# Kernel tuning notes

Measured on AMD Instinct MI355X. Metric: run time of the kernel, lower is better.

Reference implementation:

```python
import math
import jax, jax.numpy as jnp
import numpy as np

# Dimensions (scalar irreps: o3.Irreps('8x0e').dim == 8, FullyConnectedTensorProduct
# between scalar irreps reduces to a learned bilinear map with a 3D weight tensor)
N = 50000       # nodes
C = 4           # channel dim ('c' in the einsum 'nci,neio->nceo')
DI = 8          # irreps_in.dim
DE = 8          # irreps_edge_attr.dim (must equal DI for the einsum to typecheck)
DO = 8          # irreps_out.dim (must equal DI for lin2 to consume the messages)
DA = 16         # irreps_node_attr.dim
E = 400000      # edges
F_EDGE = 32     # number_of_edge_features
H = 64          # radial_neurons
NUM_NEIGHBORS = 8


def setup_inputs() -> dict:
    key = jax.random.key(0)
    ks = jax.random.split(key, 12)
    inv = lambda f: 1.0 / np.sqrt(f)
    return {
        "node_input": jax.random.normal(ks[0], (N, C, DI), jnp.float32),
        "node_attr": jax.random.normal(ks[1], (N, DA), jnp.float32),
        "edge_features": jax.random.normal(ks[2], (E, F_EDGE), jnp.float32),
        # bilinear tensor-product weights (sc, lin1, lin2)
        "W_sc": jax.random.normal(ks[3], (DI, DA, DO), jnp.float32) * inv(DI * DA),
        "W_lin1": jax.random.normal(ks[4], (DI, DA, DI), jnp.float32) * inv(DI * DA),
        "W_lin2": jax.random.normal(ks[5], (DO, DA, DO), jnp.float32) * inv(DO * DA),
        # radial MLP: Linear(F_EDGE,H) -> SiLU -> Linear(H, DI*DE*DO)
        "fc_w1": jax.random.normal(ks[6], (F_EDGE, H), jnp.float32) * inv(F_EDGE),
        "fc_b1": jnp.zeros((H,), jnp.float32),
        "fc_w2": jax.random.normal(ks[7], (H, DI * DE * DO), jnp.float32) * inv(H),
        "fc_b2": jnp.zeros((DI * DE * DO,), jnp.float32),
        "edge_src": jax.random.randint(ks[8], (E,), 0, N, jnp.int32),
        "edge_dst": jax.random.randint(ks[9], (E,), 0, N, jnp.int32),
    }


def reference(node_input, node_attr, edge_features, W_sc, W_lin1, W_lin2,
              fc_w1, fc_b1, fc_w2, fc_b2, edge_src, edge_dst):
    n_nodes = node_input.shape[0]
    # self-connection and input linear (bilinear in node feature & node attr)
    s = jnp.einsum('nci,na,iao->nco', node_input, node_attr, W_sc)      # [N,C,DO]
    x = jnp.einsum('nci,na,iaj->ncj', node_input, node_attr, W_lin1)    # [N,C,DI]
    # radial MLP -> per-edge weight tensor [E, DI, DE, DO]
    h = jax.nn.silu(edge_features @ fc_w1 + fc_b1)
    ef = (h @ fc_w2 + fc_b2).reshape(-1, DI, DE, DO)
    # gather by source, per-edge contraction (einsum 'nci,neio->nceo'):
    # contract x's irrep dim with ef axis 2, keep ef axis 1 as output dim d
    msg = jnp.einsum('eci,edio->ecdo', x[edge_src], ef)                 # [E,C,DI,DO]
    # scatter-add to destination nodes
    agg = jax.ops.segment_sum(msg, edge_dst, num_segments=n_nodes)      # [N,C,DI,DO]
    agg = agg / jnp.sqrt(jnp.asarray(NUM_NEIGHBORS, agg.dtype))
    # output linear on the last (irreps_out) axis
    x2 = jnp.einsum('ncdo,na,oap->ncdp', agg, node_attr, W_lin2)        # [N,C,DI,DO]
    c_s = math.sin(math.pi / 8.0)
    # fully-connected scalar-irrep TP -> output_mask is all ones -> c_x scalar
    c_x = math.cos(math.pi / 8.0)
    return c_s * s[:, :, None, :] + c_x * x2
```

## Files before the change

kernel.cpp:

```cpp
#include <hip/hip_runtime.h>
#include <math.h>

#define CC 4
#define FE 32
#define HH 64
#define EBS 256
#define KEXT 544
#define ASTR 69

typedef __attribute__((ext_vector_type(8))) short bf16x8;
typedef __attribute__((ext_vector_type(4))) float f32x4;

__device__ inline unsigned short f2bf(float f) {
    unsigned u = __float_as_uint(f);
    u += 0x7fffu + ((u >> 16) & 1u);
    return (unsigned short)(u >> 16);
}
__device__ inline float bf2f(unsigned short b) {
    return __uint_as_float(((unsigned)b) << 16);
}

__global__ __launch_bounds__(256) void k_nodeprep(
    const float* __restrict__ node_input, const float* __restrict__ node_attr,
    const float* __restrict__ W_lin1, const float* __restrict__ W_sc,
    const float* __restrict__ W_lin2,
    float* __restrict__ xbuf, float* __restrict__ sbuf,
    float* __restrict__ w2n_ws, int N)
{
    const float c_s = 0.3826834323650898f;
    const float c_x_scaled = 0.9238795325112867f * 0.35355339059327373f;
    int node = blockIdx.x * 4 + (threadIdx.x >> 6);
    int lane = threadIdx.x & 63;
    if (node >= N) return;

    float attr_own = (lane < 16) ? node_attr[(size_t)node * 16 + lane] : 0.f;
    float ni_own   = (lane < 32) ? node_input[(size_t)node * 32 + lane] : 0.f;

    int iw = lane >> 3, jw = lane & 7;
    float wb1 = 0.f, wbs = 0.f, w2n = 0.f;
    #pragma unroll
    for (int a = 0; a < 16; ++a) {
        float fa = __shfl(attr_own, a);
        int idx = (iw * 16 + a) * 8 + jw;
        wb1 += fa * W_lin1[idx];
        wbs += fa * W_sc[idx];
        w2n += fa * W_lin2[idx];
    }
    w2n_ws[(size_t)node * 64 + lane] = c_x_scaled * w2n;

    int c_ = (lane >> 3) & 3, jo = lane & 7;
    float xo = 0.f, so = 0.f;
    #pragma unroll
    for (int i = 0; i < 8; ++i) {
        float niv = __shfl(ni_own, c_ * 8 + i);
        xo += niv * __shfl(wb1, i * 8 + jo);
        so += niv * __shfl(wbs, i * 8 + jo);
    }
    if (lane < 32) {
        xbuf[(size_t)node * 32 + lane] = xo;
        sbuf[(size_t)node * 32 + lane] = c_s * so;
    }
}

__global__ __launch_bounds__(256) void k_hist(
    const int* __restrict__ edge_dst, int* __restrict__ counts, int E)
{
    int e = blockIdx.x * 256 + threadIdx.x;
    if (e < E) atomicAdd(&counts[edge_dst[e]], 1);
}

__global__ __launch_bounds__(1024) void k_scanA(
    const int* __restrict__ counts, int* __restrict__ offsets,
    int* __restrict__ btot, int N)
{
    __shared__ int wsum[16];
    __shared__ int wpre[16];
    int tid = threadIdx.x, wid = tid >> 6, lane = tid & 63;
    int idx = blockIdx.x * 1024 + tid;
    int v = (idx < N) ? counts[idx] : 0;
    int x = v;
    #pragma unroll
    for (int s = 1; s < 64; s <<= 1) {
        int y = __shfl_up(x, s);
        if (lane >= s) x += y;
    }
    if (lane == 63) wsum[wid] = x;
    __syncthreads();
    if (wid == 0) {
        int wv = (lane < 16) ? wsum[lane] : 0;
        int wx = wv;
        #pragma unroll
        for (int s = 1; s < 16; s <<= 1) {
            int y = __shfl_up(wx, s);
            if (lane >= s) wx += y;
        }
        if (lane < 16) wpre[lane] = wx - wv;
    }
    __syncthreads();
    int excl = wpre[wid] + (x - v);
    if (idx < N) offsets[idx] = excl;
    if (tid == 1023) btot[blockIdx.x] = excl + v;
}

__global__ __launch_bounds__(1024) void k_scanB(int* __restrict__ btot, int nb)
{
    __shared__ int wsum[16];
    __shared__ int wpre[16];
    int tid = threadIdx.x, wid = tid >> 6, lane = tid & 63;
    int v = (tid < nb) ? btot[tid] : 0;
    int x = v;
    #pragma unroll
    for (int s = 1; s < 64; s <<= 1) {
        int y = __shfl_up(x, s);
        if (lane >= s) x += y;
    }
    if (lane == 63) wsum[wid] = x;
    __syncthreads();
    if (wid == 0) {
        int wv = (lane < 16) ? wsum[lane] : 0;
        int wx = wv;
        #pragma unroll
        for (int s = 1; s < 16; s <<= 1) {
            int y = __shfl_up(wx, s);
            if (lane >= s) wx += y;
        }
        if (lane < 16) wpre[lane] = wx - wv;
    }
    __syncthreads();
    if (tid < nb) btot[tid] = wpre[wid] + (x - v);
}

__global__ __launch_bounds__(256) void k_scanC(
    int* __restrict__ offsets, const int* __restrict__ btot,
    int* __restrict__ cursor, int N)
{
    int i = blockIdx.x * 256 + threadIdx.x;
    if (i < N) {
        int o = offsets[i] + btot[i >> 10];
        offsets[i] = o;
        cursor[i] = o;
    }
}

__global__ __launch_bounds__(256) void k_fill(
    const int* __restrict__ edge_dst, const int* __restrict__ edge_src,
    int* __restrict__ cursor, int* __restrict__ srcs, int* __restrict__ epos, int E)
{
    int e = blockIdx.x * 256 + threadIdx.x;
    if (e < E) {
        int pos = atomicAdd(&cursor[edge_dst[e]], 1);
        srcs[pos] = edge_src[e];
        epos[e] = pos;
    }
}

__global__ __launch_bounds__(256) void k_prep_bfrag(
    const float* __restrict__ fc_w2, const float* __restrict__ fc_b2,
    unsigned short* __restrict__ Bfrag)
{
    int t = blockIdx.x * 256 + threadIdx.x;
    if (t >= KEXT * 64) return;
    int kappa = t >> 6, nu = t & 63;
    int d = nu >> 3, o = nu & 7;
    float val;
    if (kappa < 512)      val = fc_w2[(size_t)(kappa >> 3) * 512 + d * 64 + (kappa & 7) * 8 + o];
    else if (kappa < 520) val = fc_b2[d * 64 + (kappa & 7) * 8 + o];
    else                  val = 0.f;
    int kk = kappa >> 5;
    int lane = ((kappa >> 3) & 3) * 16 + (nu & 15);
    int ct = nu >> 4;
    int j = kappa & 7;
    Bfrag[(size_t)((kk * 4 + ct) * 64 + lane) * 8 + j] = f2bf(val);
}

__global__ __launch_bounds__(256) void k_prep_bfrag1(
    const float* __restrict__ fc_w1, unsigned short* __restrict__ Bfrag1)
{
    int t = blockIdx.x * 256 + threadIdx.x;
    if (t >= 4 * 64 * 8) return;
    int j = t & 7, l = (t >> 3) & 63, ct = t >> 9;
    int k = (l >> 4) * 8 + j;
    int n = ct * 16 + (l & 15);
    Bfrag1[t] = f2bf(fc_w1[(size_t)k * HH + n]);
}

__global__ __launch_bounds__(256) void k_hsilu(
    const float* __restrict__ edge_features,
    const unsigned short* __restrict__ Bfrag1, const float* __restrict__ fc_b1,
    const int* __restrict__ epos,
    unsigned short* __restrict__ H, int E)
{
    int wid = threadIdx.x >> 6, lane = threadIdx.x & 63;
    int e0 = (blockIdx.x * 4 + wid) * 16;
    if (e0 >= E) return;

    bf16x8 b[4];
    #pragma unroll
    for (int ct = 0; ct < 4; ++ct) {
        uint4 bv = reinterpret_cast<const uint4*>(Bfrag1)[ct * 64 + lane];
        b[ct] = *reinterpret_cast<bf16x8*>(&bv);
    }
    float bias[4];
    #pragma unroll
    for (int ct = 0; ct < 4; ++ct) bias[ct] = fc_b1[ct * 16 + (lane & 15)];

    int pr[4];
    #pragma unroll
    for (int v = 0; v < 4; ++v) {
        int r = e0 + (lane >> 4) * 4 + v;
        pr[v] = (r < E) ? epos[r] : -1;
    }

    int row = e0 + (lane & 15);
    if (row >= E) row = E - 1;
    const float4* ap = reinterpret_cast<const float4*>(
        edge_features + (size_t)row * FE + (lane >> 4) * 8);
    float4 a0 = ap[0], a1 = ap[1];
    unsigned au[4];
    au[0] = (unsigned)f2bf(a0.x) | ((unsigned)f2bf(a0.y) << 16);
    au[1] = (unsigned)f2bf(a0.z) | ((unsigned)f2bf(a0.w) << 16);
    au[2] = (unsigned)f2bf(a1.x) | ((unsigned)f2bf(a1.y) << 16);
    au[3] = (unsigned)f2bf(a1.z) | ((unsigned)f2bf(a1.w) << 16);
    bf16x8 a = *reinterpret_cast<bf16x8*>(au);

    f32x4 acc[4];
    #pragma unroll
    for (int ct = 0; ct < 4; ++ct) {
        acc[ct] = (f32x4){0.f, 0.f, 0.f, 0.f};
        acc[ct] = __builtin_amdgcn_mfma_f32_16x16x32_bf16(a, b[ct], acc[ct], 0, 0, 0);
    }

    #pragma unroll
    for (int ct = 0; ct < 4; ++ct) {
        #pragma unroll
        for (int v = 0; v < 4; ++v) {
            if (pr[v] >= 0) {
                float x = acc[ct][v] + bias[ct];
                float s = x / (1.f + __expf(-x));
                H[(size_t)pr[v] * HH + ct * 16 + (lane & 15)] = f2bf(s);
            }
        }
    }
}

__global__ __launch_bounds__(256) void k_zgemm(
    const unsigned short* __restrict__ H, const int* __restrict__ srcs,
    const int* __restrict__ offsets, const int* __restrict__ counts,
    const float* __restrict__ xin, const unsigned short* __restrict__ Bfrag,
    const float* __restrict__ sbuf, const float* __restrict__ w2n_ws,
    float* __restrict__ out, int N)
{
    __shared__ uint4 alds[16 * ASTR];
    int wid = threadIdx.x >> 6, lane = threadIdx.x & 63;
    int node = blockIdx.x * 4 + wid;
    bool valid = (node < N);

    float z[CC][8];
    #pragma unroll
    for (int c = 0; c < CC; ++c)
        #pragma unroll
        for (int i = 0; i < 8; ++i) z[c][i] = 0.f;
    float xsown = 0.f;

    int off = 0, cnt = 0;
    if (valid) { off = offsets[node]; cnt = counts[node]; }
    for (int base = 0; base < cnt; base += 64) {
        int m = (cnt - base < 64) ? (cnt - base) : 64;
        int sj = (lane < m) ? srcs[off + base + lane] : 0;
        #pragma unroll 2
        for (int j = 0; j < m; ++j) {
            int src = __shfl(sj, j);
            float hk = bf2f(H[(size_t)(off + base + j) * HH + lane]);
            const float4* xp = reinterpret_cast<const float4*>(xin + (size_t)src * 32);
            float xs[32];
            #pragma unroll
            for (int q = 0; q < 8; ++q) {
                float4 v = xp[q];
                xs[q * 4 + 0] = v.x; xs[q * 4 + 1] = v.y;
                xs[q * 4 + 2] = v.z; xs[q * 4 + 3] = v.w;
            }
            #pragma unroll
            for (int c = 0; c < CC; ++c)
                #pragma unroll
                for (int i = 0; i < 8; ++i)
                    z[c][i] += hk * xs[c * 8 + i];
            xsown += xin[(size_t)src * 32 + (lane & 31)];
        }
    }

    #pragma unroll
    for (int c = 0; c < CC; ++c) {
        uint4 pk;
        pk.x = (unsigned)f2bf(z[c][0]) | ((unsigned)f2bf(z[c][1]) << 16);
        pk.y = (unsigned)f2bf(z[c][2]) | ((unsigned)f2bf(z[c][3]) << 16);
        pk.z = (unsigned)f2bf(z[c][4]) | ((unsigned)f2bf(z[c][5]) << 16);
        pk.w = (unsigned)f2bf(z[c][6]) | ((unsigned)f2bf(z[c][7]) << 16);
        alds[(wid * 4 + c) * ASTR + lane] = pk;
    }
    float xb[8];
    #pragma unroll
    for (int i = 0; i < 8; ++i) xb[i] = __shfl(xsown, (lane & 3) * 8 + i);
    int r4 = wid * 4;
    if (lane < 4) {
        uint4 pk;
        pk.x = (unsigned)f2bf(xb[0]) | ((unsigned)f2bf(xb[1]) << 16);
        pk.y = (unsigned)f2bf(xb[2]) | ((unsigned)f2bf(xb[3]) << 16);
        pk.z = (unsigned)f2bf(xb[4]) | ((unsigned)f2bf(xb[5]) << 16);
        pk.w = (unsigned)f2bf(xb[6]) | ((unsigned)f2bf(xb[7]) << 16);
        alds[(r4 + lane) * ASTR + 64] = pk;
    } else if (lane < 16) {
        int j = lane - 4;
        uint4 zz; zz.x = 0u; zz.y = 0u; zz.z = 0u; zz.w = 0u;
        alds[(r4 + (j & 3)) * ASTR + 65 + (j >> 2)] = zz;
    }

    bf16x8 bfr[17];
    #pragma unroll
    for (int kk = 0; kk < 16; ++kk) {
        uint4 bv = reinterpret_cast<const uint4*>(Bfrag)[(kk * 4 + wid) * 64 + lane];
        bfr[kk] = *reinterpret_cast<bf16x8*>(&bv);
    }
    {
        uint4 bv = reinterpret_cast<const uint4*>(Bfrag)[(64 + wid) * 64 + lane];
        bfr[16] = *reinterpret_cast<bf16x8*>(&bv);
    }

    __syncthreads();

    f32x4 acc = (f32x4){0.f, 0.f, 0.f, 0.f};
    #pragma unroll
    for (int kk = 0; kk < 16; ++kk) {
        uint4 av = alds[(lane & 15) * ASTR + kk * 4 + (lane >> 4)];
        bf16x8 a = *reinterpret_cast<bf16x8*>(&av);
        acc = __builtin_amdgcn_mfma_f32_16x16x32_bf16(a, bfr[kk], acc, 0, 0, 0);
    }
    {
        uint4 av = alds[(lane & 15) * ASTR + 64 + (lane >> 4)];
        bf16x8 a = *reinterpret_cast<bf16x8*>(&av);
        acc = __builtin_amdgcn_mfma_f32_16x16x32_bf16(a, bfr[16], acc, 0, 0, 0);
    }

    int q = lane >> 4;
    int colc = lane & 15;
    int nq = blockIdx.x * 4 + q;
    bool vq = (nq < N);
    int realn = vq ? nq : 0;
    int col = wid * 16 + colc;
    int p = col & 7;
    int dloc8 = (colc >> 3) << 3;
    float w2r[8];
    #pragma unroll
    for (int o = 0; o < 8; ++o)
        w2r[o] = vq ? w2n_ws[(size_t)realn * 64 + o * 8 + p] : 0.f;
    #pragma unroll
    for (int v = 0; v < 4; ++v) {
        float res = 0.f;
        #pragma unroll
        for (int o = 0; o < 8; ++o)
            res += __shfl(acc[v], q * 16 + dloc8 + o) * w2r[o];
        if (vq) {
            float sv = sbuf[(size_t)realn * 32 + v * 8 + p];
            out[(size_t)(realn * 4 + v) * 64 + col] = sv + res;
        }
    }
}

__global__ __launch_bounds__(256) void k_node_out(
    const float* __restrict__ sbuf, const float* __restrict__ w2n_ws,
    float* __restrict__ out, int N)
{
    int node = blockIdx.x * 4 + (threadIdx.x >> 6);
    int lane = threadIdx.x & 63;
    if (node >= N) return;
    int d = lane >> 3, p = lane & 7;

    float w2 = w2n_ws[(size_t)node * 64 + lane];
    float s_own = sbuf[(size_t)node * 32 + (lane & 31)];

    float w2sh[8];
    #pragma unroll
    for (int o = 0; o < 8; ++o) w2sh[o] = __shfl(w2, o * 8 + p);

    float* rowp = out + (size_t)node * 256;
    #pragma unroll
    for (int c = 0; c < CC; ++c) {
        float a_own = rowp[c * 64 + lane];
        float res = 0.f;
        #pragma unroll
        for (int o = 0; o < 8; ++o)
            res += __shfl(a_own, d * 8 + o) * w2sh[o];
        float sval = __shfl(s_own, c * 8 + p);
        rowp[c * 64 + lane] = sval + res;
    }
}

__global__ __launch_bounds__(EBS) void k_edge_atomic(
    const float* __restrict__ edge_features,
    const float* __restrict__ fc_w1, const float* __restrict__ fc_b1,
    const float* __restrict__ fc_w2, const float* __restrict__ fc_b2,
    const int* __restrict__ edge_src, const int* __restrict__ edge_dst,
    const float* __restrict__ xin, float* __restrict__ agg, int E)
{
    __shared__ float hlds[HH * EBS];
    int e = blockIdx.x * EBS + threadIdx.x;
    if (e >= E) return;
    float h[HH];
    #pragma unroll
    for (int k = 0; k < HH; ++k) h[k] = fc_b1[k];
    const float4* efp = reinterpret_cast<const float4*>(edge_features + (size_t)e * FE);
    #pragma unroll
    for (int fq = 0; fq < FE / 4; ++fq) {
        float4 efv = efp[fq];
        float ev[4] = {efv.x, efv.y, efv.z, efv.w};
        #pragma unroll
        for (int fs = 0; fs < 4; ++fs) {
            float evv = ev[fs];
            const float4* w1p = reinterpret_cast<const float4*>(fc_w1 + (fq * 4 + fs) * HH);
            #pragma unroll
            for (int q = 0; q < HH / 4; ++q) {
                float4 w = w1p[q];
                h[q * 4 + 0] += evv * w.x;
                h[q * 4 + 1] += evv * w.y;
                h[q * 4 + 2] += evv * w.z;
                h[q * 4 + 3] += evv * w.w;
            }
        }
    }
    #pragma unroll
    for (int k = 0; k < HH; ++k) {
        float v = h[k];
        hlds[k * EBS + threadIdx.x] = v / (1.f + __expf(-v));
    }
    int src = edge_src[e], dst = edge_dst[e];
    float xs[32];
    const float4* xp = reinterpret_cast<const float4*>(xin + (size_t)src * 32);
    #pragma unroll
    for (int q = 0; q < 8; ++q) {
        float4 v = xp[q];
        xs[q * 4 + 0] = v.x; xs[q * 4 + 1] = v.y;
        xs[q * 4 + 2] = v.z; xs[q * 4 + 3] = v.w;
    }
    float* outp = agg + (size_t)dst * 256;
    #pragma unroll 1
    for (int d = 0; d < 8; ++d) {
        float t[64];
        const float4* b2p = reinterpret_cast<const float4*>(fc_b2 + d * 64);
        #pragma unroll
        for (int q = 0; q < 16; ++q) {
            float4 v = b2p[q];
            t[q * 4 + 0] = v.x; t[q * 4 + 1] = v.y;
            t[q * 4 + 2] = v.z; t[q * 4 + 3] = v.w;
        }
        for (int k = 0; k < HH; ++k) {
            float hv = hlds[k * EBS + threadIdx.x];
            const float4* wp = reinterpret_cast<const float4*>(fc_w2 + (size_t)k * 512 + d * 64);
            #pragma unroll
            for (int q = 0; q < 16; ++q) {
                float4 w = wp[q];
                t[q * 4 + 0] += hv * w.x;
                t[q * 4 + 1] += hv * w.y;
                t[q * 4 + 2] += hv * w.z;
                t[q * 4 + 3] += hv * w.w;
            }
        }
        #pragma unroll
        for (int c = 0; c < CC; ++c) {
            #pragma unroll
            for (int o = 0; o < 8; ++o) {
                float acc = 0.f;
                #pragma unroll
                for (int i = 0; i < 8; ++i) acc += xs[c * 8 + i] * t[i * 8 + o];
                atomicAdd(outp + c * 64 + d * 8 + o, acc);
            }
        }
    }
}

extern "C" void kernel_launch(void* const* d_in, const int* in_sizes, int n_in,
                              void* d_out, int out_size, void* d_ws, size_t ws_size,
                              hipStream_t stream)
{
    const float* node_input    = (const float*)d_in[0];
    const float* node_attr     = (const float*)d_in[1];
    const float* edge_features = (const float*)d_in[2];
    const float* W_sc          = (const float*)d_in[3];
    const float* W_lin1        = (const float*)d_in[4];
    const float* W_lin2        = (const float*)d_in[5];
    const float* fc_w1         = (const float*)d_in[6];
    const float* fc_b1         = (const float*)d_in[7];
    const float* fc_w2         = (const float*)d_in[8];
    const float* fc_b2         = (const float*)d_in[9];
    const int*   edge_src      = (const int*)d_in[10];
    const int*   edge_dst      = (const int*)d_in[11];

    const int N = in_sizes[1] / 16;
    const int E = in_sizes[10];
    const int nb = (N + 1023) / 1024;

    char* ws = (char*)d_ws;
    size_t off = 0;
    auto take = [&](size_t bytes) { char* p = ws + off; off += (bytes + 15) & ~(size_t)15; return p; };
    float* xbuf            = (float*)take((size_t)N * 32 * sizeof(float));
    float* sbuf            = (float*)take((size_t)N * 32 * sizeof(float));
    float* w2n_ws          = (float*)take((size_t)N * 64 * sizeof(float));
    int*   counts          = (int*)take((size_t)N * sizeof(int));
    int*   offsets         = (int*)take((size_t)N * sizeof(int));
    int*   cursor          = (int*)take((size_t)N * sizeof(int));
    int*   btot            = (int*)take((size_t)1024 * sizeof(int));
    int*   srcs            = (int*)take((size_t)E * sizeof(int));
    int*   epos            = (int*)take((size_t)E * sizeof(int));
    unsigned short* Bfrag  = (unsigned short*)take((size_t)17 * 4 * 64 * 8 * sizeof(unsigned short));
    unsigned short* Bfrag1 = (unsigned short*)take((size_t)4 * 64 * 8 * sizeof(unsigned short));
    unsigned short* Hbuf   = (unsigned short*)take((size_t)E * HH * sizeof(unsigned short));
    bool fast = (off <= ws_size);

    float* out = (float*)d_out;

    k_nodeprep<<<(N + 3) / 4, 256, 0, stream>>>(
        node_input, node_attr, W_lin1, W_sc, W_lin2, xbuf, sbuf, w2n_ws, N);

    if (fast) {
        hipMemsetAsync(counts, 0, (size_t)N * sizeof(int), stream);
        k_hist<<<(E + 255) / 256, 256, 0, stream>>>(edge_dst, counts, E);
        k_scanA<<<nb, 1024, 0, stream>>>(counts, offsets, btot, N);
        k_scanB<<<1, 1024, 0, stream>>>(btot, nb);
        k_scanC<<<(N + 255) / 256, 256, 0, stream>>>(offsets, btot, cursor, N);
        k_fill<<<(E + 255) / 256, 256, 0, stream>>>(edge_dst, edge_src, cursor, srcs, epos, E);
        k_prep_bfrag1<<<(4 * 64 * 8 + 255) / 256, 256, 0, stream>>>(fc_w1, Bfrag1);
        k_prep_bfrag<<<(KEXT * 64 + 255) / 256, 256, 0, stream>>>(fc_w2, fc_b2, Bfrag);
        k_hsilu<<<(E + 63) / 64, 256, 0, stream>>>(edge_features, Bfrag1, fc_b1, epos, Hbuf, E);
        k_zgemm<<<(N + 3) / 4, 256, 0, stream>>>(
            Hbuf, srcs, offsets, counts, xbuf, Bfrag, sbuf, w2n_ws, out, N);
    } else {
        hipMemsetAsync(d_out, 0, (size_t)out_size * sizeof(float), stream);
        k_edge_atomic<<<(E + EBS - 1) / EBS, EBS, 0, stream>>>(
            edge_features, fc_w1, fc_b1, fc_w2, fc_b2, edge_src, edge_dst, xbuf, out, E);
        k_node_out<<<(N + 3) / 4, 256, 0, stream>>>(sbuf, w2n_ws, out, N);
    }
}
```

Baseline: 289.8 us.

## Split per-node edge loop across two waves and move lin2 epilogue to k_node_out

k_zgemm now launches 512 threads per block, so each node gets two waves that each accumulate half of its incoming edges. The second wave hands its partial sums to the first through LDS, and the sums are rounded to bf16 on the way. The fused lin2/self-connection epilogue is removed, and the raw MFMA output is written to out for k_node_out to finish in a separate pass. The aim is more latency hiding in the gather loop, but it adds an extra full read and write of the output buffer and another kernel launch.

```diff
diff --git a/kernel.cpp b/kernel.cpp
--- a/kernel.cpp
+++ b/kernel.cpp
@@ -243,16 +243,17 @@
     }
 }
 
-__global__ __launch_bounds__(256) void k_zgemm(
+__global__ __launch_bounds__(512) void k_zgemm(
     const unsigned short* __restrict__ H, const int* __restrict__ srcs,
     const int* __restrict__ offsets, const int* __restrict__ counts,
     const float* __restrict__ xin, const unsigned short* __restrict__ Bfrag,
-    const float* __restrict__ sbuf, const float* __restrict__ w2n_ws,
     float* __restrict__ out, int N)
 {
     __shared__ uint4 alds[16 * ASTR];
+    __shared__ float xsp[4][64];
     int wid = threadIdx.x >> 6, lane = threadIdx.x & 63;
-    int node = blockIdx.x * 4 + wid;
+    int nslot = wid & 3, half = wid >> 2;
+    int node = blockIdx.x * 4 + nslot;
     bool valid = (node < N);
 
     float z[CC][8];
@@ -264,13 +265,17 @@
 
     int off = 0, cnt = 0;
     if (valid) { off = offsets[node]; cnt = counts[node]; }
-    for (int base = 0; base < cnt; base += 64) {
-        int m = (cnt - base < 64) ? (cnt - base) : 64;
-        int sj = (lane < m) ? srcs[off + base + lane] : 0;
+    int c0 = cnt >> 1;
+    int mystart = off + (half ? c0 : 0);
+    int mycnt = half ? (cnt - c0) : c0;
+
+    for (int base = 0; base < mycnt; base += 64) {
+        int m = (mycnt - base < 64) ? (mycnt - base) : 64;
+        int sj = (lane < m) ? srcs[mystart + base + lane] : 0;
         #pragma unroll 2
         for (int j = 0; j < m; ++j) {
             int src = __shfl(sj, j);
-            float hk = bf2f(H[(size_t)(off + base + j) * HH + lane]);
+            float hk = bf2f(H[(size_t)(mystart + base + j) * HH + lane]);
             const float4* xp = reinterpret_cast<const float4*>(xin + (size_t)src * 32);
             float xs[32];
             #pragma unroll
@@ -288,79 +293,92 @@
         }
     }
 
-    #pragma unroll
-    for (int c = 0; c < CC; ++c) {
-        uint4 pk;
-        pk.x = (unsigned)f2bf(z[c][0]) | ((unsigned)f2bf(z[c][1]) << 16);
-        pk.y = (unsigned)f2bf(z[c][2]) | ((unsigned)f2bf(z[c][3]) << 16);
-        pk.z = (unsigned)f2bf(z[c][4]) | ((unsigned)f2bf(z[c][5]) << 16);
-        pk.w = (unsigned)f2bf(z[c][6]) | ((unsigned)f2bf(z[c][7]) << 16);
-        alds[(wid * 4 + c) * ASTR + lane] = pk;
-    }
-    float xb[8];
-    #pragma unroll
-    for (int i = 0; i < 8; ++i) xb[i] = __shfl(xsown, (lane & 3) * 8 + i);
-    int r4 = wid * 4;
-    if (lane < 4) {
-        uint4 pk;
-        pk.x = (unsigned)f2bf(xb[0]) | ((unsigned)f2bf(xb[1]) << 16);
-        pk.y = (unsigned)f2bf(xb[2]) | ((unsigned)f2bf(xb[3]) << 16);
-        pk.z = (unsigned)f2bf(xb[4]) | ((unsigned)f2bf(xb[5]) << 16);
-        pk.w = (unsigned)f2bf(xb[6]) | ((unsigned)f2bf(xb[7]) << 16);
-        alds[(r4 + lane) * ASTR + 64] = pk;
-    } else if (lane < 16) {
-        int j = lane - 4;
-        uint4 zz; zz.x = 0u; zz.y = 0u; zz.z = 0u; zz.w = 0u;
-        alds[(r4 + (j & 3)) * ASTR + 65 + (j >> 2)] = zz;
-    }
+    if (half) {
+        #pragma unroll
+        for (int c = 0; c < CC; ++c) {
+            uint4 pk;
+            pk.x = (unsigned)f2bf(z[c][0]) | ((unsigned)f2bf(z[c][1]) << 16);
+            pk.y = (unsigned)f2bf(z[c][2]) | ((unsigned)f2bf(z[c][3]) << 16);
+            pk.z = (unsigned)f2bf(z[c][4]) | ((unsigned)f2bf(z[c][5]) << 16);
+            pk.w = (unsigned)f2bf(z[c][6]) | ((unsigned)f2bf(z[c][7]) << 16);
+            alds[(nslot * 4 + c) * ASTR + lane] = pk;
+        }
+        xsp[nslot][lane] = xsown;
+    }
+    __syncthreads();
 
     bf16x8 bfr[17];
-    #pragma unroll
-    for (int kk = 0; kk < 16; ++kk) {
-        uint4 bv = reinterpret_cast<const uint4*>(Bfrag)[(kk * 4 + wid) * 64 + lane];
-        bfr[kk] = *reinterpret_cast<bf16x8*>(&bv);
-    }
-    {
-        uint4 bv = reinterpret_cast<const uint4*>(Bfrag)[(64 + wid) * 64 + lane];
-        bfr[16] = *reinterpret_cast<bf16x8*>(&bv);
-    }
-
+    if (!half) {
+        #pragma unroll
+        for (int c = 0; c < CC; ++c) {
+            uint4 pv = alds[(nslot * 4 + c) * ASTR + lane];
+            unsigned w0 = pv.x, w1 = pv.y, w2 = pv.z, w3 = pv.w;
+            z[c][0] += bf2f((unsigned short)(w0 & 0xffffu));
+            z[c][1] += bf2f((unsigned short)(w0 >> 16));
+            z[c][2] += bf2f((unsigned short)(w1 & 0xffffu));
+            z[c][3] += bf2f((unsigned short)(w1 >> 16));
+            z[c][4] += bf2f((unsigned short)(w2 & 0xffffu));
+            z[c][5] += bf2f((unsigned short)(w2 >> 16));
+            z[c][6] += bf2f((unsigned short)(w3 & 0xffffu));
+            z[c][7] += bf2f((unsigned short)(w3 >> 16));
+            uint4 pk;
+            pk.x = (unsigned)f2bf(z[c][0]) | ((unsigned)f2bf(z[c][1]) << 16);
+            pk.y = (unsigned)f2bf(z[c][2]) | ((unsigned)f2bf(z[c][3]) << 16);
+            pk.z = (unsigned)f2bf(z[c][4]) | ((unsigned)f2bf(z[c][5]) << 16);
+            pk.w = (unsigned)f2bf(z[c][6]) | ((unsigned)f2bf(z[c][7]) << 16);
+            alds[(nslot * 4 + c) * ASTR + lane] = pk;
+        }
+        xsown += xsp[nslot][lane];
+
+        float xb[8];
+        #pragma unroll
+        for (int i = 0; i < 8; ++i) xb[i] = __shfl(xsown, (lane & 3) * 8 + i);
+        int r4 = nslot * 4;
+        if (lane < 4) {
+            uint4 pk;
+            pk.x = (unsigned)f2bf(xb[0]) | ((unsigned)f2bf(xb[1]) << 16);
+            pk.y = (unsigned)f2bf(xb[2]) | ((unsigned)f2bf(xb[3]) << 16);
+            pk.z = (unsigned)f2bf(xb[4]) | ((unsigned)f2bf(xb[5]) << 16);
+            pk.w = (unsigned)f2bf(xb[6]) | ((unsigned)f2bf(xb[7]) << 16);
+            alds[(r4 + lane) * ASTR + 64] = pk;
+        } else if (lane < 16) {
+            int j = lane - 4;
+            uint4 zz; zz.x = 0u; zz.y = 0u; zz.z = 0u; zz.w = 0u;
+            alds[(r4 + (j & 3)) * ASTR + 65 + (j >> 2)] = zz;
+        }
+
+        #pragma unroll
+        for (int kk = 0; kk < 16; ++kk) {
+            uint4 bv = reinterpret_cast<const uint4*>(Bfrag)[(kk * 4 + nslot) * 64 + lane];
+            bfr[kk] = *reinterpret_cast<bf16x8*>(&bv);
+        }
+        {
+            uint4 bv = reinterpret_cast<const uint4*>(Bfrag)[(64 + nslot) * 64 + lane];
+            bfr[16] = *reinterpret_cast<bf16x8*>(&bv);
+        }
+    }
     __syncthreads();
 
-    f32x4 acc = (f32x4){0.f, 0.f, 0.f, 0.f};
-    #pragma unroll
-    for (int kk = 0; kk < 16; ++kk) {
-        uint4 av = alds[(lane & 15) * ASTR + kk * 4 + (lane >> 4)];
-        bf16x8 a = *reinterpret_cast<bf16x8*>(&av);
-        acc = __builtin_amdgcn_mfma_f32_16x16x32_bf16(a, bfr[kk], acc, 0, 0, 0);
-    }
-    {
-        uint4 av = alds[(lane & 15) * ASTR + 64 + (lane >> 4)];
-        bf16x8 a = *reinterpret_cast<bf16x8*>(&av);
-        acc = __builtin_amdgcn_mfma_f32_16x16x32_bf16(a, bfr[16], acc, 0, 0, 0);
-    }
-
-    int q = lane >> 4;
-    int colc = lane & 15;
-    int nq = blockIdx.x * 4 + q;
-    bool vq = (nq < N);
-    int realn = vq ? nq : 0;
-    int col = wid * 16 + colc;
-    int p = col & 7;
-    int dloc8 = (colc >> 3) << 3;
-    float w2r[8];
-    #pragma unroll
-    for (int o = 0; o < 8; ++o)
-        w2r[o] = vq ? w2n_ws[(size_t)realn * 64 + o * 8 + p] : 0.f;
-    #pragma unroll
-    for (int v = 0; v < 4; ++v) {
-        float res = 0.f;
-        #pragma unroll
-        for (int o = 0; o < 8; ++o)
-            res += __shfl(acc[v], q * 16 + dloc8 + o) * w2r[o];
-        if (vq) {
-            float sv = sbuf[(size_t)realn * 32 + v * 8 + p];
-            out[(size_t)(realn * 4 + v) * 64 + col] = sv + res;
+    if (!half) {
+        f32x4 acc = (f32x4){0.f, 0.f, 0.f, 0.f};
+        #pragma unroll
+        for (int kk = 0; kk < 16; ++kk) {
+            uint4 av = alds[(lane & 15) * ASTR + kk * 4 + (lane >> 4)];
+            bf16x8 a = *reinterpret_cast<bf16x8*>(&av);
+            acc = __builtin_amdgcn_mfma_f32_16x16x32_bf16(a, bfr[kk], acc, 0, 0, 0);
+        }
+        {
+            uint4 av = alds[(lane & 15) * ASTR + 64 + (lane >> 4)];
+            bf16x8 a = *reinterpret_cast<bf16x8*>(&av);
+            acc = __builtin_amdgcn_mfma_f32_16x16x32_bf16(a, bfr[16], acc, 0, 0, 0);
+        }
+        int rbase = blockIdx.x * 16;
+        int M = N * 4;
+        #pragma unroll
+        for (int v = 0; v < 4; ++v) {
+            int r = rbase + (lane >> 4) * 4 + v;
+            if (r < M)
+                out[(size_t)r * 64 + nslot * 16 + (lane & 15)] = acc[v];
         }
     }
 }
@@ -529,8 +547,9 @@
         k_prep_bfrag1<<<(4 * 64 * 8 + 255) / 256, 256, 0, stream>>>(fc_w1, Bfrag1);
         k_prep_bfrag<<<(KEXT * 64 + 255) / 256, 256, 0, stream>>>(fc_w2, fc_b2, Bfrag);
         k_hsilu<<<(E + 63) / 64, 256, 0, stream>>>(edge_features, Bfrag1, fc_b1, epos, Hbuf, E);
-        k_zgemm<<<(N + 3) / 4, 256, 0, stream>>>(
-            Hbuf, srcs, offsets, counts, xbuf, Bfrag, sbuf, w2n_ws, out, N);
+        k_zgemm<<<(N + 3) / 4, 512, 0, stream>>>(
+            Hbuf, srcs, offsets, counts, xbuf, Bfrag, out, N);
+        k_node_out<<<(N + 3) / 4, 256, 0, stream>>>(sbuf, w2n_ws, out, N);
     } else {
         hipMemsetAsync(d_out, 0, (size_t)out_size * sizeof(float), stream);
         k_edge_atomic<<<(E + EBS - 1) / EBS, EBS, 0, stream>>>(
```

New measurement: 328.7 us. +13.4%, slower.

## Pre-gather source features into edge-sorted buffer and split output linear

Applied to the files above, without the earlier changes.

Adds a kernel that copies each edge's gathered source node features into a contiguous CSR-ordered buffer, so the aggregation kernel streams them instead of doing indirect loads. The aggregation kernel now writes raw aggregated values and leaves the lin2 projection plus self-connection to the existing node-output kernel. This removes random gathers and epilogue work from the main kernel. In exchange it adds a 51 MB write and read pass, two extra launches, and an extra round trip of the output array.

```diff
diff --git a/kernel.cpp b/kernel.cpp
--- a/kernel.cpp
+++ b/kernel.cpp
@@ -152,6 +152,20 @@
         srcs[pos] = edge_src[e];
         epos[e] = pos;
     }
+}
+
+__global__ __launch_bounds__(256) void k_xgather(
+    const int* __restrict__ srcs, const float* __restrict__ xin,
+    float* __restrict__ xg, int E)
+{
+    int t = blockIdx.x * 256 + threadIdx.x;
+    if (t >= E * 4) return;
+    int pos = t >> 2, q = t & 3;
+    int src = srcs[pos];
+    const float4* xp = reinterpret_cast<const float4*>(xin + (size_t)src * 32 + q * 8);
+    float4 a = xp[0], b = xp[1];
+    float4* op = reinterpret_cast<float4*>(xg + (size_t)pos * 32 + q * 8);
+    op[0] = a; op[1] = b;
 }
 
 __global__ __launch_bounds__(256) void k_prep_bfrag(
@@ -244,10 +258,9 @@
 }
 
 __global__ __launch_bounds__(256) void k_zgemm(
-    const unsigned short* __restrict__ H, const int* __restrict__ srcs,
+    const unsigned short* __restrict__ H, const float* __restrict__ xg,
     const int* __restrict__ offsets, const int* __restrict__ counts,
-    const float* __restrict__ xin, const unsigned short* __restrict__ Bfrag,
-    const float* __restrict__ sbuf, const float* __restrict__ w2n_ws,
+    const unsigned short* __restrict__ Bfrag,
     float* __restrict__ out, int N)
 {
     __shared__ uint4 alds[16 * ASTR];
@@ -264,28 +277,24 @@
 
     int off = 0, cnt = 0;
     if (valid) { off = offsets[node]; cnt = counts[node]; }
-    for (int base = 0; base < cnt; base += 64) {
-        int m = (cnt - base < 64) ? (cnt - base) : 64;
-        int sj = (lane < m) ? srcs[off + base + lane] : 0;
-        #pragma unroll 2
-        for (int j = 0; j < m; ++j) {
-            int src = __shfl(sj, j);
-            float hk = bf2f(H[(size_t)(off + base + j) * HH + lane]);
-            const float4* xp = reinterpret_cast<const float4*>(xin + (size_t)src * 32);
-            float xs[32];
+    #pragma unroll 2
+    for (int j = 0; j < cnt; ++j) {
+        size_t pos = (size_t)(off + j);
+        float hk = bf2f(H[pos * HH + lane]);
+        const float4* xp = reinterpret_cast<const float4*>(xg + pos * 32);
+        float xs[32];
+        #pragma unroll
+        for (int q = 0; q < 8; ++q) {
+            float4 v = xp[q];
+            xs[q * 4 + 0] = v.x; xs[q * 4 + 1] = v.y;
+            xs[q * 4 + 2] = v.z; xs[q * 4 + 3] = v.w;
+        }
+        #pragma unroll
+        for (int c = 0; c < CC; ++c)
             #pragma unroll
-            for (int q = 0; q < 8; ++q) {
-                float4 v = xp[q];
-                xs[q * 4 + 0] = v.x; xs[q * 4 + 1] = v.y;
-                xs[q * 4 + 2] = v.z; xs[q * 4 + 3] = v.w;
-            }
-            #pragma unroll
-            for (int c = 0; c < CC; ++c)
-                #pragma unroll
-                for (int i = 0; i < 8; ++i)
-                    z[c][i] += hk * xs[c * 8 + i];
-            xsown += xin[(size_t)src * 32 + (lane & 31)];
-        }
+            for (int i = 0; i < 8; ++i)
+                z[c][i] += hk * xs[c * 8 + i];
+        xsown += xg[pos * 32 + (lane & 31)];
     }
 
     #pragma unroll
@@ -340,28 +349,13 @@
         acc = __builtin_amdgcn_mfma_f32_16x16x32_bf16(a, bfr[16], acc, 0, 0, 0);
     }
 
-    int q = lane >> 4;
-    int colc = lane & 15;
-    int nq = blockIdx.x * 4 + q;
-    bool vq = (nq < N);
-    int realn = vq ? nq : 0;
-    int col = wid * 16 + colc;
-    int p = col & 7;
-    int dloc8 = (colc >> 3) << 3;
-    float w2r[8];
-    #pragma unroll
-    for (int o = 0; o < 8; ++o)
-        w2r[o] = vq ? w2n_ws[(size_t)realn * 64 + o * 8 + p] : 0.f;
+    int rbase = blockIdx.x * 16;
+    int M = N * 4;
     #pragma unroll
     for (int v = 0; v < 4; ++v) {
-        float res = 0.f;
-        #pragma unroll
-        for (int o = 0; o < 8; ++o)
-            res += __shfl(acc[v], q * 16 + dloc8 + o) * w2r[o];
-        if (vq) {
-            float sv = sbuf[(size_t)realn * 32 + v * 8 + p];
-            out[(size_t)(realn * 4 + v) * 64 + col] = sv + res;
-        }
+        int r = rbase + (lane >> 4) * 4 + v;
+        if (r < M)
+            out[(size_t)r * 64 + wid * 16 + (lane & 15)] = acc[v];
     }
 }
 
@@ -512,6 +506,7 @@
     unsigned short* Bfrag  = (unsigned short*)take((size_t)17 * 4 * 64 * 8 * sizeof(unsigned short));
     unsigned short* Bfrag1 = (unsigned short*)take((size_t)4 * 64 * 8 * sizeof(unsigned short));
     unsigned short* Hbuf   = (unsigned short*)take((size_t)E * HH * sizeof(unsigned short));
+    float* xg              = (float*)take((size_t)E * 32 * sizeof(float));
     bool fast = (off <= ws_size);
 
     float* out = (float*)d_out;
@@ -529,8 +524,10 @@
         k_prep_bfrag1<<<(4 * 64 * 8 + 255) / 256, 256, 0, stream>>>(fc_w1, Bfrag1);
         k_prep_bfrag<<<(KEXT * 64 + 255) / 256, 256, 0, stream>>>(fc_w2, fc_b2, Bfrag);
         k_hsilu<<<(E + 63) / 64, 256, 0, stream>>>(edge_features, Bfrag1, fc_b1, epos, Hbuf, E);
+        k_xgather<<<(E * 4 + 255) / 256, 256, 0, stream>>>(srcs, xbuf, xg, E);
         k_zgemm<<<(N + 3) / 4, 256, 0, stream>>>(
-            Hbuf, srcs, offsets, counts, xbuf, Bfrag, sbuf, w2n_ws, out, N);
+            Hbuf, xg, offsets, counts, Bfrag, out, N);
+        k_node_out<<<(N + 3) / 4, 256, 0, stream>>>(sbuf, w2n_ws, out, N);
     } else {
         hipMemsetAsync(d_out, 0, (size_t)out_size * sizeof(float), stream);
         k_edge_atomic<<<(E + EBS - 1) / EBS, EBS, 0, stream>>>(
```

Result: no change. 290.3 us (+0.2%).
